# Performance work log

Hardware: AMD Instinct MI355X
Metric: run time of the kernel (lower is better)

The kernel has to match this reference:

```python
import jax, jax.numpy as jnp
import numpy as np

NUM_HEADS = 16
EPS = 1e-6
ROPE_THETA = 10000.0


def _rmsnorm_fp32(x, w):
    # RMSNorm computed in fp32, scale by learned weight (per head_dim)
    xf = x.astype(jnp.float32)
    var = jnp.mean(xf * xf, axis=-1, keepdims=True)
    return (xf * jax.lax.rsqrt(var + EPS) * w.astype(jnp.float32)).astype(x.dtype)


def _rope_3d_angles(T, H, W, head_dim):
    # split head_dim across (t,h,w) axes; all parts even
    dh = 2 * ((head_dim // 3) // 2)
    dw = dh
    dt = head_dim - dh - dw

    def axis_ang(L, d):
        inv = 1.0 / (ROPE_THETA ** (jnp.arange(0, d, 2, dtype=jnp.float32) / d))
        return jnp.arange(L, dtype=jnp.float32)[:, None] * inv[None, :]  # [L, d//2]

    at = axis_ang(T, dt)  # [T, dt/2]
    ah = axis_ang(H, dh)  # [H, dh/2]
    aw = axis_ang(W, dw)  # [W, dw/2]
    # broadcast to [T,H,W, head_dim//2] then flatten to [N, head_dim//2]
    at_g = jnp.broadcast_to(at[:, None, None, :], (T, H, W, dt // 2))
    ah_g = jnp.broadcast_to(ah[None, :, None, :], (T, H, W, dh // 2))
    aw_g = jnp.broadcast_to(aw[None, None, :, :], (T, H, W, dw // 2))
    ang = jnp.concatenate([at_g, ah_g, aw_g], axis=-1).reshape(T * H * W, head_dim // 2)
    return jnp.cos(ang), jnp.sin(ang)


def _apply_rope(x, cos, sin):
    # x: [B,Hh,N,D]; cos/sin: [N, D/2]; interleaved complex-pair rotation
    xr = x[..., 0::2]
    xi = x[..., 1::2]
    c = cos[None, None, :, :]
    s = sin[None, None, :, :]
    out_r = xr * c - xi * s
    out_i = xr * s + xi * c
    return jnp.stack([out_r, out_i], axis=-1).reshape(x.shape)


def setup_inputs() -> dict:
    key = jax.random.key(0)
    ks = jax.random.split(key, 7)
    dim, hd = 2048, 128
    x = jax.random.normal(ks[0], (1, 2048, dim), dtype=jnp.float32)
    qkv_w = jax.random.normal(ks[1], (3 * dim, dim), dtype=jnp.float32) * (dim ** -0.5)
    qkv_b = jax.random.normal(ks[2], (3 * dim,), dtype=jnp.float32) * 0.02
    proj_w = jax.random.normal(ks[3], (dim, dim), dtype=jnp.float32) * (dim ** -0.5)
    proj_b = jax.random.normal(ks[4], (dim,), dtype=jnp.float32) * 0.02
    q_norm_w = jnp.ones((hd,), dtype=jnp.float32)
    k_norm_w = jnp.ones((hd,), dtype=jnp.float32)
    return {"x": x, "qkv_w": qkv_w, "qkv_b": qkv_b, "proj_w": proj_w,
            "proj_b": proj_b, "q_norm_w": q_norm_w, "k_norm_w": k_norm_w,
            "t_dim": 8, "h_dim": 16, "w_dim": 16}


def reference(x, qkv_w, qkv_b, proj_w, proj_b, q_norm_w, k_norm_w, t_dim, h_dim, w_dim):
    B, N, C = x.shape
    Hh = NUM_HEADS
    D = C // Hh
    scale = D ** -0.5
    # QKV projection (torch Linear: x @ W.T + b)
    qkv = x @ qkv_w.T + qkv_b                      # [B,N,3C]
    qkv = qkv.reshape(B, N, 3, Hh, D).transpose(2, 0, 3, 1, 4)  # [3,B,Hh,N,D]
    q, k, v = qkv[0], qkv[1], qkv[2]
    q = _rmsnorm_fp32(q, q_norm_w)
    k = _rmsnorm_fp32(k, k_norm_w)
    cos, sin = _rope_3d_angles(t_dim, h_dim, w_dim, D)
    q = _apply_rope(q, cos, sin)
    k = _apply_rope(k, cos, sin)
    # SDPA (non-causal)
    scores = jnp.einsum('bhqd,bhkd->bhqk', q, k) * scale
    attn = jax.nn.softmax(scores, axis=-1)
    out = jnp.einsum('bhqk,bhkd->bhqd', attn, v)   # [B,Hh,N,D]
    out = out.transpose(0, 2, 1, 3).reshape(B, N, C)
    return out @ proj_w.T + proj_b
```

## Files before the change

### kernel.cpp

```cpp
#include <hip/hip_runtime.h>
#include <hip/hip_bf16.h>
#include <cstdint>
#include <cstddef>

typedef __attribute__((ext_vector_type(8))) short bf16x8;
typedef __attribute__((ext_vector_type(4))) float f32x4;
typedef __attribute__((ext_vector_type(16))) float f32x16;

#define AS1 __attribute__((address_space(1)))
#define AS3 __attribute__((address_space(3)))

__device__ __forceinline__ void gload_lds16(const void* g, void* l) {
  __builtin_amdgcn_global_load_lds((const AS1 void*)g, (AS3 void*)l, 16, 0, 0);
}

__device__ __forceinline__ unsigned short f2bf(float x) {
  __hip_bfloat16 h = __float2bfloat16(x);
  return __builtin_bit_cast(unsigned short, h);
}
__device__ __forceinline__ float bf2f(unsigned short u) {
  return __builtin_bit_cast(float, (unsigned int)u << 16);
}

__global__ __launch_bounds__(256) void k_cvt_bf16(const float* __restrict__ in,
                                                  unsigned short* __restrict__ out,
                                                  int n4) {
  int i = blockIdx.x * 256 + threadIdx.x;
  const int stride = gridDim.x * 256;
  for (; i < n4; i += stride) {
    float4 v = reinterpret_cast<const float4*>(in)[i];
    ushort4 o;
    o.x = f2bf(v.x); o.y = f2bf(v.y); o.z = f2bf(v.z); o.w = f2bf(v.w);
    reinterpret_cast<ushort4*>(out)[i] = o;
  }
}

__global__ __launch_bounds__(256) void k_rope_tab(float* __restrict__ cosT,
                                                  float* __restrict__ sinT,
                                                  const int* __restrict__ hdim,
                                                  const int* __restrict__ wdim) {
  int idx = blockIdx.x * 256 + threadIdx.x;
  if (idx >= 2048 * 64) return;
  const int n = idx >> 6, j = idx & 63;
  const int H = *hdim, W = *wdim;
  const int w = n % W;
  const int rem = n / W;
  const int h = rem % H;
  const int t = rem / H;
  float pos, i2, d;
  if (j < 22)      { pos = (float)t; i2 = (float)(2 * j);        d = 44.f; }
  else if (j < 43) { pos = (float)h; i2 = (float)(2 * (j - 22)); d = 42.f; }
  else             { pos = (float)w; i2 = (float)(2 * (j - 43)); d = 42.f; }
  const float ang = pos * powf(10000.0f, -i2 / d);
  cosT[idx] = cosf(ang);
  sinT[idx] = sinf(ang);
}

__global__ __launch_bounds__(512, 2) void k_gemm256(const unsigned short* __restrict__ A,
                                                    const unsigned short* __restrict__ B,
                                                    const float* __restrict__ bias,
                                                    unsigned short* __restrict__ C,
                                                    int M, int N, int K) {
  __shared__ __align__(16) char lds[131072];
  const int tid = threadIdx.x;
  const int lane = tid & 63;
  const int wid = tid >> 6;
  const int wr = wid >> 2, wc = wid & 3;

  const int nbx = N >> 8;
  const int xcd = blockIdx.x & 7;
  const int t = blockIdx.x >> 3;
  const int cchunk = nbx >> 3;
  const int swz = (t & 7) * nbx + xcd * cchunk + (t >> 3);
  const int by = swz / nbx, bx = swz % nbx;
  const int row0 = by * 256, col0 = bx * 256;
  const int NT = K >> 6;

  auto stage_slot = [&](const unsigned short* src, int grow0, int kcol0, char* slot) {
#pragma unroll
    for (int r = 0; r < 2; ++r) {
      const int off = r * 8192 + tid * 16;
      const int pair = off >> 7;
      const int un = (off & 127) ^ ((pair & 7) << 4);
      const int grow = pair * 2 + (un >> 6);
      gload_lds16(src + (size_t)(grow0 + grow) * K + kcol0 + ((un & 63) >> 1),
                  slot + r * 8192 + wid * 1024);
    }
  };
  auto frag = [&](const char* slot, int r, int kb) -> bf16x8 {
    return *reinterpret_cast<const bf16x8*>(
        slot + (r >> 1) * 128 + ((((r & 1) << 6) + kb) ^ (((r >> 1) & 7) << 4)));
  };

  f32x4 acc[8][4];
#pragma unroll
  for (int i = 0; i < 8; ++i)
#pragma unroll
    for (int j = 0; j < 4; ++j) acc[i][j] = (f32x4){0.f, 0.f, 0.f, 0.f};

  stage_slot(A, row0, 0,  lds);
  stage_slot(B, col0, 0,  lds + 65536);
  stage_slot(A, row0, 32, lds + 16384);
  stage_slot(B, col0, 32, lds + 65536 + 16384);
  asm volatile("s_waitcnt vmcnt(4)" ::: "memory");
  __builtin_amdgcn_s_barrier();

  const int kb = (lane >> 4) << 4;
  for (int j = 0; j < NT; ++j) {
    const int b = j & 1, bp = b ^ 1;
    const char* A0 = lds + (2 * b + 0) * 16384;
    const char* A1 = lds + (2 * b + 1) * 16384;
    const char* B0 = lds + 65536 + (2 * b + 0) * 16384;
    const char* B1 = lds + 65536 + (2 * b + 1) * 16384;
    char* pA0 = lds + (2 * bp + 0) * 16384;
    char* pA1 = lds + (2 * bp + 1) * 16384;
    char* pB0 = lds + 65536 + (2 * bp + 0) * 16384;
    char* pB1 = lds + 65536 + (2 * bp + 1) * 16384;
    const bool pf = (j + 1 < NT);
    const int kn = (j + 1) * 64;
    bf16x8 af[8], bq[2];

#pragma unroll
    for (int rf = 0; rf < 8; ++rf) af[rf] = frag(A0, wr * 128 + rf * 16 + (lane & 15), kb);
#pragma unroll
    for (int cf = 0; cf < 2; ++cf) bq[cf] = frag(B0, wc * 64 + cf * 16 + (lane & 15), kb);
    if (pf) stage_slot(A, row0, kn, pA0);
    __builtin_amdgcn_s_barrier();
    __builtin_amdgcn_s_setprio(1);
#pragma unroll
    for (int rf = 0; rf < 8; ++rf)
#pragma unroll
      for (int cf = 0; cf < 2; ++cf)
        acc[rf][cf] = __builtin_amdgcn_mfma_f32_16x16x32_bf16(af[rf], bq[cf], acc[rf][cf], 0, 0, 0);
    __builtin_amdgcn_s_setprio(0);
    __builtin_amdgcn_s_barrier();

#pragma unroll
    for (int cf = 0; cf < 2; ++cf) bq[cf] = frag(B0, wc * 64 + (cf + 2) * 16 + (lane & 15), kb);
    if (pf) stage_slot(B, col0, kn, pB0);
    if (pf) asm volatile("s_waitcnt vmcnt(4)" ::: "memory");
    else    asm volatile("s_waitcnt vmcnt(0)" ::: "memory");
    __builtin_amdgcn_s_barrier();
    __builtin_amdgcn_s_setprio(1);
#pragma unroll
    for (int rf = 0; rf < 8; ++rf)
#pragma unroll
      for (int cf = 0; cf < 2; ++cf)
        acc[rf][cf + 2] = __builtin_amdgcn_mfma_f32_16x16x32_bf16(af[rf], bq[cf], acc[rf][cf + 2], 0, 0, 0);
    __builtin_amdgcn_s_setprio(0);
    __builtin_amdgcn_s_barrier();

#pragma unroll
    for (int rf = 0; rf < 8; ++rf) af[rf] = frag(A1, wr * 128 + rf * 16 + (lane & 15), kb);
#pragma unroll
    for (int cf = 0; cf < 2; ++cf) bq[cf] = frag(B1, wc * 64 + cf * 16 + (lane & 15), kb);
    if (pf) stage_slot(A, row0, kn + 32, pA1);
    __builtin_amdgcn_s_barrier();
    __builtin_amdgcn_s_setprio(1);
#pragma unroll
    for (int rf = 0; rf < 8; ++rf)
#pragma unroll
      for (int cf = 0; cf < 2; ++cf)
        acc[rf][cf] = __builtin_amdgcn_mfma_f32_16x16x32_bf16(af[rf], bq[cf], acc[rf][cf], 0, 0, 0);
    __builtin_amdgcn_s_setprio(0);
    __builtin_amdgcn_s_barrier();

#pragma unroll
    for (int cf = 0; cf < 2; ++cf) bq[cf] = frag(B1, wc * 64 + (cf + 2) * 16 + (lane & 15), kb);
    if (pf) stage_slot(B, col0, kn + 32, pB1);
    if (pf) asm volatile("s_waitcnt vmcnt(4)" ::: "memory");
    __builtin_amdgcn_s_barrier();
    __builtin_amdgcn_s_setprio(1);
#pragma unroll
    for (int rf = 0; rf < 8; ++rf)
#pragma unroll
      for (int cf = 0; cf < 2; ++cf)
        acc[rf][cf + 2] = __builtin_amdgcn_mfma_f32_16x16x32_bf16(af[rf], bq[cf], acc[rf][cf + 2], 0, 0, 0);
    __builtin_amdgcn_s_setprio(0);
    __builtin_amdgcn_s_barrier();
  }

#pragma unroll
  for (int fr = 0; fr < 8; ++fr)
#pragma unroll
    for (int fc = 0; fc < 4; ++fc) {
      const int col = col0 + wc * 64 + fc * 16 + (lane & 15);
      const float bv = bias[col];
#pragma unroll
      for (int jj = 0; jj < 4; ++jj) {
        const int row = row0 + wr * 128 + fr * 16 + (lane >> 4) * 4 + jj;
        C[(size_t)row * N + col] = f2bf(acc[fr][fc][jj] + bv);
      }
    }
}

__global__ __launch_bounds__(256) void k_gemm_bt_sk(const unsigned short* __restrict__ A,
                                                    const unsigned short* __restrict__ B,
                                                    float* __restrict__ Cp,
                                                    int M, int N, int K, int KS) {
  __shared__ __align__(16) unsigned short As[128 * 32];
  __shared__ __align__(16) unsigned short Bs[128 * 32];
  const int lane = threadIdx.x & 63;
  const int wid  = threadIdx.x >> 6;
  const int wr = wid >> 1, wc = wid & 1;
  const int rowA0 = blockIdx.y * 128;
  const int rowB0 = blockIdx.x * 128;
  const int k0 = blockIdx.z * KS;

  f32x4 acc[4][4];
#pragma unroll
  for (int i = 0; i < 4; ++i)
#pragma unroll
    for (int j = 0; j < 4; ++j) acc[i][j] = (f32x4){0.f, 0.f, 0.f, 0.f};

  for (int kt = k0; kt < k0 + KS; kt += 32) {
#pragma unroll
    for (int i = 0; i < 2; ++i) {
      const int c = i * 4 + wid;
      const int off = c * 1024 + lane * 16;
      const int row = off >> 6;
      const int col = (off & 63) >> 1;
      gload_lds16(A + (size_t)(rowA0 + row) * K + kt + col, (char*)As + c * 1024);
      gload_lds16(B + (size_t)(rowB0 + row) * K + kt + col, (char*)Bs + c * 1024);
    }
    __syncthreads();
    bf16x8 af[4], bfr[4];
#pragma unroll
    for (int mi = 0; mi < 4; ++mi)
      af[mi] = *reinterpret_cast<const bf16x8*>(
          &As[(wr * 64 + mi * 16 + (lane & 15)) * 32 + (lane >> 4) * 8]);
#pragma unroll
    for (int ni = 0; ni < 4; ++ni)
      bfr[ni] = *reinterpret_cast<const bf16x8*>(
          &Bs[(wc * 64 + ni * 16 + (lane & 15)) * 32 + (lane >> 4) * 8]);
#pragma unroll
    for (int mi = 0; mi < 4; ++mi)
#pragma unroll
      for (int ni = 0; ni < 4; ++ni)
        acc[mi][ni] = __builtin_amdgcn_mfma_f32_16x16x32_bf16(af[mi], bfr[ni], acc[mi][ni], 0, 0, 0);
    __syncthreads();
  }

  float* Cz = Cp + (size_t)blockIdx.z * M * N;
#pragma unroll
  for (int mi = 0; mi < 4; ++mi)
#pragma unroll
    for (int ni = 0; ni < 4; ++ni) {
      const int col = rowB0 + wc * 64 + ni * 16 + (lane & 15);
#pragma unroll
      for (int j = 0; j < 4; ++j) {
        const int row = rowA0 + wr * 64 + mi * 16 + (lane >> 4) * 4 + j;
        Cz[(size_t)row * N + col] = acc[mi][ni][j];
      }
    }
}

__global__ __launch_bounds__(256) void k_addbias(const float* __restrict__ Cp,
                                                 const float* __restrict__ bias,
                                                 float* __restrict__ out) {
  const int i = blockIdx.x * 256 + threadIdx.x;
  const float4 a = reinterpret_cast<const float4*>(Cp)[i];
  const float4 b = reinterpret_cast<const float4*>(Cp + 2048ull * 2048)[i];
  const float4 bv = reinterpret_cast<const float4*>(bias)[i & 511];
  float4 o;
  o.x = a.x + b.x + bv.x; o.y = a.y + b.y + bv.y;
  o.z = a.z + b.z + bv.z; o.w = a.w + b.w + bv.w;
  reinterpret_cast<float4*>(out)[i] = o;
}

__global__ __launch_bounds__(256) void k_qk_post(const unsigned short* __restrict__ qkv,
                                                 const float* __restrict__ qw,
                                                 const float* __restrict__ kw,
                                                 const float* __restrict__ cosT,
                                                 const float* __restrict__ sinT,
                                                 unsigned short* __restrict__ qo,
                                                 unsigned short* __restrict__ ko) {
  const int lane = threadIdx.x & 63;
  const int wid = threadIdx.x >> 6;
  const int pair = blockIdx.x * 4 + wid;
  const int n = pair >> 4, h = pair & 15;
  const float c = cosT[n * 64 + lane];
  const float s = sinT[n * 64 + lane];
#pragma unroll
  for (int sq = 0; sq < 2; ++sq) {
    const unsigned short* src = qkv + (size_t)n * 6144 + sq * 2048 + h * 128;
    const unsigned int vp = reinterpret_cast<const unsigned int*>(src)[lane];
    const float vx = bf2f((unsigned short)(vp & 0xffff));
    const float vy = bf2f((unsigned short)(vp >> 16));
    float ss = vx * vx + vy * vy;
#pragma unroll
    for (int m = 1; m < 64; m <<= 1) ss += __shfl_xor(ss, m, 64);
    const float r = rsqrtf(ss * (1.0f / 128.0f) + 1e-6f);
    float2 wv = reinterpret_cast<const float2*>(sq == 0 ? qw : kw)[lane];
    const float xr = vx * r * wv.x;
    const float xi = vy * r * wv.y;
    float orr = xr * c - xi * s;
    float oi  = xr * s + xi * c;
    if (sq == 0) { orr *= 0.08838834764831845f; oi *= 0.08838834764831845f; }
    unsigned short* dst = (sq == 0 ? qo : ko) + ((size_t)h * 2048 + n) * 128 + 2 * lane;
    const unsigned int pk = (unsigned int)f2bf(orr) | ((unsigned int)f2bf(oi) << 16);
    *reinterpret_cast<unsigned int*>(dst) = pk;
  }
}

__global__ __launch_bounds__(256) void k_v_tr(const unsigned short* __restrict__ qkv,
                                              unsigned short* __restrict__ vt2) {
  __shared__ __align__(16) unsigned short tile[64][136];
  const int h = blockIdx.y;
  const int n0 = blockIdx.x * 64;
  const int t = threadIdx.x;
  {
    const int row = t >> 2;
    const int c0 = (t & 3) * 32;
    const unsigned short* src = qkv + (size_t)(n0 + row) * 6144 + 4096 + h * 128 + c0;
#pragma unroll
    for (int j = 0; j < 32; j += 8)
      *reinterpret_cast<bf16x8*>(&tile[row][c0 + j]) =
          *reinterpret_cast<const bf16x8*>(src + j);
  }
  __syncthreads();
#pragma unroll
  for (int g4 = 0; g4 < 4; ++g4) {
    const int g = g4 * 256 + t;
    const int c = g >> 8;
    const int dblk = (g >> 6) & 3;
    const int p = g & 63;
    const int d = dblk * 32 + (p & 31);
    const int hi = p >> 5;
    bf16x8 o;
#pragma unroll
    for (int e = 0; e < 8; ++e) o[e] = (short)tile[c * 16 + hi * 8 + e][d];
    const size_t oidx = ((((size_t)h * 128 + (n0 >> 4) + c) * 4 + dblk) * 64 + p) * 8;
    *reinterpret_cast<bf16x8*>(vt2 + oidx) = o;
  }
}

__global__ __launch_bounds__(256) void k_fattn(const unsigned short* __restrict__ q,
                                               const unsigned short* __restrict__ k,
                                               const unsigned short* __restrict__ vt2,
                                               unsigned short* __restrict__ Onorm,
                                               float* __restrict__ lseb) {
  __shared__ __align__(16) unsigned short Ks[3][64 * 128];
  __shared__ __align__(16) unsigned short Ps[4][32][68];
  const int lane = threadIdx.x & 63;
  const int wid = threadIdx.x >> 6;
  const int hi2 = lane >> 5;
  const int ql = lane & 31;
  const int bid = blockIdx.x;
  const int h = bid & 15;
  const int qb = (bid >> 4) & 15;
  const int ksp = bid >> 8;
  const int q0 = qb * 128 + wid * 32;
  const int kbase = ksp * 1024;

  auto stageK = [&](int buf, int kt2) {
#pragma unroll
    for (int r = 0; r < 4; ++r) {
      const int off = r * 4096 + (wid * 64 + lane) * 16;
      const int row = off >> 8;
      const int colb = (off & 255) ^ ((row & 15) << 4);
      gload_lds16(k + ((size_t)h * 2048 + kbase + kt2 * 64 + row) * 128 + (colb >> 1),
                  (char*)Ks[buf] + r * 4096 + wid * 1024);
    }
  };

  bf16x8 qf[8];
  {
    const unsigned short* qp = q + ((size_t)h * 2048 + q0 + ql) * 128 + hi2 * 8;
#pragma unroll
    for (int c = 0; c < 8; ++c) qf[c] = *reinterpret_cast<const bf16x8*>(qp + c * 16);
  }
  f32x16 O[4];
#pragma unroll
  for (int i = 0; i < 4; ++i)
#pragma unroll
    for (int j = 0; j < 16; ++j) O[i][j] = 0.f;
  float m = -1e30f, l = 0.f;

  stageK(0, 0);
  stageK(1, 1);
  asm volatile("s_waitcnt vmcnt(4)" ::: "memory");
  __builtin_amdgcn_s_barrier();

  const int kswz = (lane & 15) << 4;
  for (int kt = 0; kt < 16; ++kt) {
    const int cur = kt % 3;

    f32x16 s0, s1;
#pragma unroll
    for (int j = 0; j < 16; ++j) { s0[j] = 0.f; s1[j] = 0.f; }
    __builtin_amdgcn_s_setprio(1);
#pragma unroll
    for (int c = 0; c < 8; ++c) {
      bf16x8 a0 = *reinterpret_cast<const bf16x8*>(
          (const char*)Ks[cur] + ql * 256 + ((c * 32 + hi2 * 16) ^ kswz));
      s0 = __builtin_amdgcn_mfma_f32_32x32x16_bf16(a0, qf[c], s0, 0, 0, 0);
    }
#pragma unroll
    for (int c = 0; c < 8; ++c) {
      bf16x8 a1 = *reinterpret_cast<const bf16x8*>(
          (const char*)Ks[cur] + (32 + ql) * 256 + ((c * 32 + hi2 * 16) ^ kswz));
      s1 = __builtin_amdgcn_mfma_f32_32x32x16_bf16(a1, qf[c], s1, 0, 0, 0);
    }
    __builtin_amdgcn_s_setprio(0);

    float mt = s0[0];
#pragma unroll
    for (int j = 1; j < 16; ++j) mt = fmaxf(mt, s0[j]);
#pragma unroll
    for (int j = 0; j < 16; ++j) mt = fmaxf(mt, s1[j]);
    mt = fmaxf(mt, __shfl_xor(mt, 32, 64));

    if (!__all(mt <= m + 8.0f)) {
      const float mn = fmaxf(m, mt);
      const float al = __expf(m - mn);
      m = mn;
      l *= al;
#pragma unroll
      for (int i = 0; i < 4; ++i)
#pragma unroll
        for (int j = 0; j < 16; ++j) O[i][j] *= al;
    }
    float rs = 0.f;
#pragma unroll
    for (int j = 0; j < 16; ++j) {
      s0[j] = __expf(s0[j] - m); rs += s0[j];
      s1[j] = __expf(s1[j] - m); rs += s1[j];
    }
    rs += __shfl_xor(rs, 32, 64);
    l += rs;

#pragma unroll
    for (int a = 0; a < 4; ++a) {
      uint2 w0, w1;
      w0.x = (unsigned)f2bf(s0[a * 4 + 0]) | ((unsigned)f2bf(s0[a * 4 + 1]) << 16);
      w0.y = (unsigned)f2bf(s0[a * 4 + 2]) | ((unsigned)f2bf(s0[a * 4 + 3]) << 16);
      w1.x = (unsigned)f2bf(s1[a * 4 + 0]) | ((unsigned)f2bf(s1[a * 4 + 1]) << 16);
      w1.y = (unsigned)f2bf(s1[a * 4 + 2]) | ((unsigned)f2bf(s1[a * 4 + 3]) << 16);
      *reinterpret_cast<uint2*>(&Ps[wid][ql][a * 8 + hi2 * 4]) = w0;
      *reinterpret_cast<uint2*>(&Ps[wid][ql][32 + a * 8 + hi2 * 4]) = w1;
    }
    bf16x8 pf[4];
#pragma unroll
    for (int c2 = 0; c2 < 4; ++c2) {
      uint2 u0 = *reinterpret_cast<const uint2*>(&Ps[wid][ql][c2 * 16 + hi2 * 8]);
      uint2 u1 = *reinterpret_cast<const uint2*>(&Ps[wid][ql][c2 * 16 + hi2 * 8 + 4]);
      union { uint4 u; bf16x8 v; } pu;
      pu.u.x = u0.x; pu.u.y = u0.y; pu.u.z = u1.x; pu.u.w = u1.y;
      pf[c2] = pu.v;
    }

    const int cg0 = (kbase >> 4) + kt * 4;
    __builtin_amdgcn_s_setprio(1);
#pragma unroll
    for (int dblk = 0; dblk < 4; ++dblk) {
#pragma unroll
      for (int c2 = 0; c2 < 4; ++c2) {
        bf16x8 va = *reinterpret_cast<const bf16x8*>(
            vt2 + ((((size_t)h * 128 + cg0 + c2) * 4 + dblk) * 64 + lane) * 8);
        O[dblk] = __builtin_amdgcn_mfma_f32_32x32x16_bf16(va, pf[c2], O[dblk], 0, 0, 0);
      }
    }
    __builtin_amdgcn_s_setprio(0);

    if (kt + 2 < 16) stageK((kt + 2) % 3, kt + 2);
    if (kt + 1 < 16) {
      asm volatile("s_waitcnt vmcnt(4)" ::: "memory");
      __builtin_amdgcn_s_barrier();
    }
  }

  const float rl = 1.0f / l;
  const int n = q0 + ql;
  unsigned short* ob = Onorm + (((size_t)(ksp * 16 + h) * 2048) + n) * 128;
#pragma unroll
  for (int dblk = 0; dblk < 4; ++dblk)
#pragma unroll
    for (int a = 0; a < 4; ++a) {
      uint2 w;
      w.x = (unsigned)f2bf(O[dblk][a * 4 + 0] * rl) | ((unsigned)f2bf(O[dblk][a * 4 + 1] * rl) << 16);
      w.y = (unsigned)f2bf(O[dblk][a * 4 + 2] * rl) | ((unsigned)f2bf(O[dblk][a * 4 + 3] * rl) << 16);
      *reinterpret_cast<uint2*>(ob + dblk * 32 + a * 8 + hi2 * 4) = w;
    }
  if (hi2 == 0)
    lseb[(size_t)(ksp * 16 + h) * 2048 + n] = m + logf(l);
}

__global__ __launch_bounds__(256) void k_merge(const unsigned short* __restrict__ Onorm,
                                               const float* __restrict__ lseb,
                                               unsigned short* __restrict__ att) {
  const int idx = blockIdx.x * 256 + threadIdx.x;
  const int n = idx >> 8;
  const int r = idx & 255;
  const int h = r >> 4;
  const int d0 = (r & 15) * 8;
  const float l0 = lseb[(size_t)h * 2048 + n];
  const float l1 = lseb[(size_t)(16 + h) * 2048 + n];
  const float M = fmaxf(l0, l1);
  float w0 = __expf(l0 - M), w1 = __expf(l1 - M);
  const float inv = 1.0f / (w0 + w1);
  w0 *= inv; w1 *= inv;
  const bf16x8 o0 = *reinterpret_cast<const bf16x8*>(
      Onorm + ((size_t)h * 2048 + n) * 128 + d0);
  const bf16x8 o1 = *reinterpret_cast<const bf16x8*>(
      Onorm + ((size_t)(16 + h) * 2048 + n) * 128 + d0);
  bf16x8 o;
#pragma unroll
  for (int e = 0; e < 8; ++e)
    o[e] = (short)f2bf(bf2f((unsigned short)o0[e]) * w0 + bf2f((unsigned short)o1[e]) * w1);
  *reinterpret_cast<bf16x8*>(att + (size_t)n * 2048 + h * 128 + d0) = o;
}

extern "C" void kernel_launch(void* const* d_in, const int* in_sizes, int n_in,
                              void* d_out, int out_size, void* d_ws, size_t ws_size,
                              hipStream_t stream) {
  (void)in_sizes; (void)n_in; (void)out_size; (void)ws_size;
  const float* x      = (const float*)d_in[0];
  const float* qkv_w  = (const float*)d_in[1];
  const float* qkv_b  = (const float*)d_in[2];
  const float* proj_w = (const float*)d_in[3];
  const float* proj_b = (const float*)d_in[4];
  const float* q_nw   = (const float*)d_in[5];
  const float* k_nw   = (const float*)d_in[6];
  const int* h_dim    = (const int*)d_in[8];
  const int* w_dim    = (const int*)d_in[9];
  float* out = (float*)d_out;

  char* ws = (char*)d_ws;
  size_t off = 0;
  auto carve = [&](size_t bytes) -> void* {
    void* p = ws + off;
    off += (bytes + 255) & ~(size_t)255;
    return p;
  };
  unsigned short* x_bf   = (unsigned short*)carve(2048ull * 2048 * 2);
  unsigned short* w1_bf  = (unsigned short*)carve(6144ull * 2048 * 2);
  unsigned short* w2_bf  = (unsigned short*)carve(2048ull * 2048 * 2);
  unsigned short* qkvb   = (unsigned short*)carve(2048ull * 6144 * 2);
  unsigned short* q_bf   = (unsigned short*)carve(16ull * 2048 * 128 * 2);
  unsigned short* k_bf   = (unsigned short*)carve(16ull * 2048 * 128 * 2);
  unsigned short* vt2_bf = (unsigned short*)carve(16ull * 2048 * 128 * 2);
  unsigned short* att_bf = (unsigned short*)carve(2048ull * 2048 * 2);
  unsigned short* on_bf  = (unsigned short*)carve(2ull * 16 * 2048 * 128 * 2);
  float*          lseb   = (float*)carve(2ull * 16 * 2048 * 4);
  float*          projp  = (float*)carve(2ull * 2048 * 2048 * 4);
  float*          cosT   = (float*)carve(2048ull * 64 * 4);
  float*          sinT   = (float*)carve(2048ull * 64 * 4);

  hipLaunchKernelGGL(k_cvt_bf16, dim3(2048), dim3(256), 0, stream, x, x_bf, 2048 * 2048 / 4);
  hipLaunchKernelGGL(k_cvt_bf16, dim3(2048), dim3(256), 0, stream, qkv_w, w1_bf, 6144 * 2048 / 4);
  hipLaunchKernelGGL(k_cvt_bf16, dim3(2048), dim3(256), 0, stream, proj_w, w2_bf, 2048 * 2048 / 4);
  hipLaunchKernelGGL(k_rope_tab, dim3(512), dim3(256), 0, stream, cosT, sinT, h_dim, w_dim);
  hipLaunchKernelGGL(k_gemm256, dim3(192), dim3(512), 0, stream,
                     x_bf, w1_bf, qkv_b, qkvb, 2048, 6144, 2048);
  hipLaunchKernelGGL(k_qk_post, dim3(8192), dim3(256), 0, stream,
                     qkvb, q_nw, k_nw, cosT, sinT, q_bf, k_bf);
  hipLaunchKernelGGL(k_v_tr, dim3(32, 16), dim3(256), 0, stream, qkvb, vt2_bf);
  hipLaunchKernelGGL(k_fattn, dim3(512), dim3(256), 0, stream,
                     q_bf, k_bf, vt2_bf, on_bf, lseb);
  hipLaunchKernelGGL(k_merge, dim3(2048), dim3(256), 0, stream, on_bf, lseb, att_bf);
  hipLaunchKernelGGL(k_gemm_bt_sk, dim3(16, 16, 2), dim3(256), 0, stream,
                     att_bf, w2_bf, projp, 2048, 2048, 2048, 1024);
  hipLaunchKernelGGL(k_addbias, dim3(4096), dim3(256), 0, stream, projp, proj_b, out);
}
```

Before: 207.5 us.

## Retile QKV GEMM to 128x192 blocks with 256 threads and 512 workgroups

Replaces the 256x256-tile QKV GEMM (192 blocks of 512 threads) with a 128x192 tile using 4 waves, giving 512 blocks so the 256 CUs are better filled and fewer stay idle in a partial wave. The pipeline is restructured into two k-halves per iteration, each with a single barrier phase that stages A and B together, and the grid mapping is simplified to an XCD-based column grouping. The trade-off is lower arithmetic intensity per tile and more global traffic, and the 192-wide B tile needs three staging loads per thread.

```diff
diff --git a/kernel.cpp b/kernel.cpp
--- a/kernel.cpp
+++ b/kernel.cpp
@@ -56,35 +56,44 @@
   sinT[idx] = sinf(ang);
 }
 
-__global__ __launch_bounds__(512, 2) void k_gemm256(const unsigned short* __restrict__ A,
+__global__ __launch_bounds__(256, 2) void k_gemmQKV(const unsigned short* __restrict__ A,
                                                     const unsigned short* __restrict__ B,
                                                     const float* __restrict__ bias,
                                                     unsigned short* __restrict__ C,
                                                     int M, int N, int K) {
-  __shared__ __align__(16) char lds[131072];
+  __shared__ __align__(16) char lds[81920];
   const int tid = threadIdx.x;
   const int lane = tid & 63;
   const int wid = tid >> 6;
-  const int wr = wid >> 2, wc = wid & 3;
-
-  const int nbx = N >> 8;
+  const int wr = wid >> 1, wc = wid & 1;
+
   const int xcd = blockIdx.x & 7;
   const int t = blockIdx.x >> 3;
-  const int cchunk = nbx >> 3;
-  const int swz = (t & 7) * nbx + xcd * cchunk + (t >> 3);
-  const int by = swz / nbx, bx = swz % nbx;
-  const int row0 = by * 256, col0 = bx * 256;
+  const int bx = xcd * 4 + (t & 3);
+  const int by = t >> 2;
+  const int row0 = by * 128, col0 = bx * 192;
   const int NT = K >> 6;
 
-  auto stage_slot = [&](const unsigned short* src, int grow0, int kcol0, char* slot) {
+  auto stageA = [&](int grow0, int kcol0, char* slot) {
 #pragma unroll
     for (int r = 0; r < 2; ++r) {
-      const int off = r * 8192 + tid * 16;
+      const int off = r * 4096 + tid * 16;
       const int pair = off >> 7;
       const int un = (off & 127) ^ ((pair & 7) << 4);
       const int grow = pair * 2 + (un >> 6);
-      gload_lds16(src + (size_t)(grow0 + grow) * K + kcol0 + ((un & 63) >> 1),
-                  slot + r * 8192 + wid * 1024);
+      gload_lds16(A + (size_t)(grow0 + grow) * K + kcol0 + ((un & 63) >> 1),
+                  slot + r * 4096 + wid * 1024);
+    }
+  };
+  auto stageB = [&](int grow0, int kcol0, char* slot) {
+#pragma unroll
+    for (int r = 0; r < 3; ++r) {
+      const int off = r * 4096 + tid * 16;
+      const int pair = off >> 7;
+      const int un = (off & 127) ^ ((pair & 7) << 4);
+      const int grow = pair * 2 + (un >> 6);
+      gload_lds16(B + (size_t)(grow0 + grow) * K + kcol0 + ((un & 63) >> 1),
+                  slot + r * 4096 + wid * 1024);
     }
   };
   auto frag = [&](const char* slot, int r, int kb) -> bf16x8 {
@@ -92,103 +101,71 @@
         slot + (r >> 1) * 128 + ((((r & 1) << 6) + kb) ^ (((r >> 1) & 7) << 4)));
   };
 
-  f32x4 acc[8][4];
-#pragma unroll
-  for (int i = 0; i < 8; ++i)
-#pragma unroll
-    for (int j = 0; j < 4; ++j) acc[i][j] = (f32x4){0.f, 0.f, 0.f, 0.f};
-
-  stage_slot(A, row0, 0,  lds);
-  stage_slot(B, col0, 0,  lds + 65536);
-  stage_slot(A, row0, 32, lds + 16384);
-  stage_slot(B, col0, 32, lds + 65536 + 16384);
-  asm volatile("s_waitcnt vmcnt(4)" ::: "memory");
+  f32x4 acc[4][6];
+#pragma unroll
+  for (int i = 0; i < 4; ++i)
+#pragma unroll
+    for (int j = 0; j < 6; ++j) acc[i][j] = (f32x4){0.f, 0.f, 0.f, 0.f};
+
+  stageA(row0, 0,  lds);
+  stageB(col0, 0,  lds + 16384);
+  stageA(row0, 32, lds + 8192);
+  stageB(col0, 32, lds + 28672);
+  asm volatile("s_waitcnt vmcnt(5)" ::: "memory");
   __builtin_amdgcn_s_barrier();
 
   const int kb = (lane >> 4) << 4;
   for (int j = 0; j < NT; ++j) {
     const int b = j & 1, bp = b ^ 1;
-    const char* A0 = lds + (2 * b + 0) * 16384;
-    const char* A1 = lds + (2 * b + 1) * 16384;
-    const char* B0 = lds + 65536 + (2 * b + 0) * 16384;
-    const char* B1 = lds + 65536 + (2 * b + 1) * 16384;
-    char* pA0 = lds + (2 * bp + 0) * 16384;
-    char* pA1 = lds + (2 * bp + 1) * 16384;
-    char* pB0 = lds + 65536 + (2 * bp + 0) * 16384;
-    char* pB1 = lds + 65536 + (2 * bp + 1) * 16384;
+    const char* base = lds + b * 40960;
+    char* pbase = lds + bp * 40960;
     const bool pf = (j + 1 < NT);
     const int kn = (j + 1) * 64;
-    bf16x8 af[8], bq[2];
-
-#pragma unroll
-    for (int rf = 0; rf < 8; ++rf) af[rf] = frag(A0, wr * 128 + rf * 16 + (lane & 15), kb);
-#pragma unroll
-    for (int cf = 0; cf < 2; ++cf) bq[cf] = frag(B0, wc * 64 + cf * 16 + (lane & 15), kb);
-    if (pf) stage_slot(A, row0, kn, pA0);
-    __builtin_amdgcn_s_barrier();
-    __builtin_amdgcn_s_setprio(1);
-#pragma unroll
-    for (int rf = 0; rf < 8; ++rf)
-#pragma unroll
-      for (int cf = 0; cf < 2; ++cf)
-        acc[rf][cf] = __builtin_amdgcn_mfma_f32_16x16x32_bf16(af[rf], bq[cf], acc[rf][cf], 0, 0, 0);
-    __builtin_amdgcn_s_setprio(0);
-    __builtin_amdgcn_s_barrier();
-
-#pragma unroll
-    for (int cf = 0; cf < 2; ++cf) bq[cf] = frag(B0, wc * 64 + (cf + 2) * 16 + (lane & 15), kb);
-    if (pf) stage_slot(B, col0, kn, pB0);
-    if (pf) asm volatile("s_waitcnt vmcnt(4)" ::: "memory");
+    bf16x8 af[4], bq[6];
+
+#pragma unroll
+    for (int fr = 0; fr < 4; ++fr) af[fr] = frag(base, wr * 64 + fr * 16 + (lane & 15), kb);
+#pragma unroll
+    for (int fc = 0; fc < 6; ++fc) bq[fc] = frag(base + 16384, wc * 96 + fc * 16 + (lane & 15), kb);
+    if (pf) { stageA(row0, kn, pbase); stageB(col0, kn, pbase + 16384); }
+    if (pf) asm volatile("s_waitcnt vmcnt(5)" ::: "memory");
     else    asm volatile("s_waitcnt vmcnt(0)" ::: "memory");
     __builtin_amdgcn_s_barrier();
     __builtin_amdgcn_s_setprio(1);
 #pragma unroll
-    for (int rf = 0; rf < 8; ++rf)
-#pragma unroll
-      for (int cf = 0; cf < 2; ++cf)
-        acc[rf][cf + 2] = __builtin_amdgcn_mfma_f32_16x16x32_bf16(af[rf], bq[cf], acc[rf][cf + 2], 0, 0, 0);
+    for (int fr = 0; fr < 4; ++fr)
+#pragma unroll
+      for (int fc = 0; fc < 6; ++fc)
+        acc[fr][fc] = __builtin_amdgcn_mfma_f32_16x16x32_bf16(af[fr], bq[fc], acc[fr][fc], 0, 0, 0);
     __builtin_amdgcn_s_setprio(0);
     __builtin_amdgcn_s_barrier();
 
 #pragma unroll
-    for (int rf = 0; rf < 8; ++rf) af[rf] = frag(A1, wr * 128 + rf * 16 + (lane & 15), kb);
-#pragma unroll
-    for (int cf = 0; cf < 2; ++cf) bq[cf] = frag(B1, wc * 64 + cf * 16 + (lane & 15), kb);
-    if (pf) stage_slot(A, row0, kn + 32, pA1);
+    for (int fr = 0; fr < 4; ++fr) af[fr] = frag(base + 8192, wr * 64 + fr * 16 + (lane & 15), kb);
+#pragma unroll
+    for (int fc = 0; fc < 6; ++fc) bq[fc] = frag(base + 28672, wc * 96 + fc * 16 + (lane & 15), kb);
+    if (pf) { stageA(row0, kn + 32, pbase + 8192); stageB(col0, kn + 32, pbase + 28672); }
+    if (pf) asm volatile("s_waitcnt vmcnt(5)" ::: "memory");
     __builtin_amdgcn_s_barrier();
     __builtin_amdgcn_s_setprio(1);
 #pragma unroll
-    for (int rf = 0; rf < 8; ++rf)
-#pragma unroll
-      for (int cf = 0; cf < 2; ++cf)
-        acc[rf][cf] = __builtin_amdgcn_mfma_f32_16x16x32_bf16(af[rf], bq[cf], acc[rf][cf], 0, 0, 0);
+    for (int fr = 0; fr < 4; ++fr)
+#pragma unroll
+      for (int fc = 0; fc < 6; ++fc)
+        acc[fr][fc] = __builtin_amdgcn_mfma_f32_16x16x32_bf16(af[fr], bq[fc], acc[fr][fc], 0, 0, 0);
     __builtin_amdgcn_s_setprio(0);
     __builtin_amdgcn_s_barrier();
-
-#pragma unroll
-    for (int cf = 0; cf < 2; ++cf) bq[cf] = frag(B1, wc * 64 + (cf + 2) * 16 + (lane & 15), kb);
-    if (pf) stage_slot(B, col0, kn + 32, pB1);
-    if (pf) asm volatile("s_waitcnt vmcnt(4)" ::: "memory");
-    __builtin_amdgcn_s_barrier();
-    __builtin_amdgcn_s_setprio(1);
-#pragma unroll
-    for (int rf = 0; rf < 8; ++rf)
-#pragma unroll
-      for (int cf = 0; cf < 2; ++cf)
-        acc[rf][cf + 2] = __builtin_amdgcn_mfma_f32_16x16x32_bf16(af[rf], bq[cf], acc[rf][cf + 2], 0, 0, 0);
-    __builtin_amdgcn_s_setprio(0);
-    __builtin_amdgcn_s_barrier();
-  }
-
-#pragma unroll
-  for (int fr = 0; fr < 8; ++fr)
-#pragma unroll
-    for (int fc = 0; fc < 4; ++fc) {
-      const int col = col0 + wc * 64 + fc * 16 + (lane & 15);
+  }
+
+#pragma unroll
+  for (int fr = 0; fr < 4; ++fr)
+#pragma unroll
+    for (int fc = 0; fc < 6; ++fc) {
+      const int col = col0 + wc * 96 + fc * 16 + (lane & 15);
       const float bv = bias[col];
 #pragma unroll
       for (int jj = 0; jj < 4; ++jj) {
-        const int row = row0 + wr * 128 + fr * 16 + (lane >> 4) * 4 + jj;
+        const int row = row0 + wr * 64 + fr * 16 + (lane >> 4) * 4 + jj;
         C[(size_t)row * N + col] = f2bf(acc[fr][fc][jj] + bv);
       }
     }
@@ -551,7 +528,7 @@
   hipLaunchKernelGGL(k_cvt_bf16, dim3(2048), dim3(256), 0, stream, qkv_w, w1_bf, 6144 * 2048 / 4);
   hipLaunchKernelGGL(k_cvt_bf16, dim3(2048), dim3(256), 0, stream, proj_w, w2_bf, 2048 * 2048 / 4);
   hipLaunchKernelGGL(k_rope_tab, dim3(512), dim3(256), 0, stream, cosT, sinT, h_dim, w_dim);
-  hipLaunchKernelGGL(k_gemm256, dim3(192), dim3(512), 0, stream,
+  hipLaunchKernelGGL(k_gemmQKV, dim3(512), dim3(256), 0, stream,
                      x_bf, w1_bf, qkv_b, qkvb, 2048, 6144, 2048);
   hipLaunchKernelGGL(k_qk_post, dim3(8192), dim3(256), 0, stream,
                      qkvb, q_nw, k_nw, cosT, sinT, q_bf, k_bf);
```

Result: no change. 204.2 us (-1.6%).
